# Kernel tuning notes

Measured on AMD Instinct MI355X. Metric: run time of the kernel, lower is better.

Reference implementation:

```python
import jax, jax.numpy as jnp
import numpy as np

EPS = 1e-5
GROUPS = 16


def _deform_conv_gn(input, offset, mask, weight, bias, gamma, beta):
    # Modulated deformable conv v2 (k=3, stride=1, pad=1) + GroupNorm(16).
    B, C, H, W = input.shape
    Co = weight.shape[0]
    K = 9
    # kernel taps relative to center (pad=1 cancels the -1 origin shift)
    ky = jnp.repeat(jnp.arange(3) - 1, 3).astype(input.dtype)   # [9]
    kx = jnp.tile(jnp.arange(3) - 1, 3).astype(input.dtype)     # [9]
    off = offset.reshape(B, K, 2, H, W)                          # (dy, dx) per tap
    dy, dx = off[:, :, 0], off[:, :, 1]                          # [B,9,H,W]
    y = jnp.arange(H, dtype=input.dtype)[None, None, :, None] + ky[None, :, None, None] + dy
    x = jnp.arange(W, dtype=input.dtype)[None, None, None, :] + kx[None, :, None, None] + dx
    y0 = jnp.floor(y)
    x0 = jnp.floor(x)
    flat = input.reshape(B, C, H * W)

    def corner(yc, xc):
        # zero-padded bilinear corner gather -> [B,C,9,H,W]
        valid = ((yc >= 0) & (yc < H) & (xc >= 0) & (xc < W)).astype(input.dtype)
        yi = jnp.clip(yc, 0, H - 1).astype(jnp.int32)
        xi = jnp.clip(xc, 0, W - 1).astype(jnp.int32)
        idx = (yi * W + xi).reshape(B, -1)
        g = jax.vmap(lambda im, ix: jnp.take(im, ix, axis=1))(flat, idx)
        return g.reshape(B, C, K, H, W) * valid[:, None]

    wy1 = y - y0
    wx1 = x - x0
    wy0 = 1.0 - wy1
    wx0 = 1.0 - wx1
    val = (corner(y0, x0) * (wy0 * wx0)[:, None]
           + corner(y0, x0 + 1.0) * (wy0 * wx1)[:, None]
           + corner(y0 + 1.0, x0) * (wy1 * wx0)[:, None]
           + corner(y0 + 1.0, x0 + 1.0) * (wy1 * wx1)[:, None])
    cols = val * mask[:, None]                                   # modulation [B,C,9,H,W]
    out = jnp.einsum('bckhw,ock->bohw', cols, weight.reshape(Co, C, K))
    out = out + bias[None, :, None, None]
    # GroupNorm(16)
    g = out.reshape(B, GROUPS, Co // GROUPS, H, W)
    mu = g.mean(axis=(2, 3, 4), keepdims=True)
    var = g.var(axis=(2, 3, 4), keepdims=True)
    g = (g - mu) * jax.lax.rsqrt(var + EPS)
    return g.reshape(B, Co, H, W) * gamma[None, :, None, None] + beta[None, :, None, None]


def setup_inputs() -> dict:
    key = jax.random.key(0)
    k1, k2, k3, k4 = jax.random.split(key, 4)
    B, C, Co, H, W = 4, 256, 256, 64, 64
    return {
        'input': jax.random.normal(k1, (B, C, H, W), dtype=jnp.float32),
        'offset': jax.random.normal(k2, (B, 18, H, W), dtype=jnp.float32),
        'mask': jax.random.uniform(k3, (B, 9, H, W), dtype=jnp.float32),
        'weight': jax.random.normal(k4, (Co, C, 3, 3), dtype=jnp.float32) * 0.02,
        'bias': jnp.zeros((Co,), dtype=jnp.float32),
        'gamma': jnp.ones((Co,), dtype=jnp.float32),
        'beta': jnp.zeros((Co,), dtype=jnp.float32),
    }


def reference(input, offset, mask, weight, bias, gamma, beta):
    return _deform_conv_gn(input, offset, mask, weight, bias, gamma, beta)
```

## Files before the change

### kernel.cpp

```cpp
#include <hip/hip_runtime.h>

typedef __attribute__((ext_vector_type(8))) short short8;
typedef __attribute__((ext_vector_type(4))) float f32x4;

#define Bsz 4
#define Cin 256
#define Cout 256
#define Hh 64
#define Ww 64
#define HW 4096
#define NG 16
#define EPSV 1e-5f

#define CSTR 40

static __device__ __forceinline__ unsigned f2bf(float f) {
    unsigned u = __float_as_uint(f);
    return (u + 0x7fffu + ((u >> 16) & 1u)) >> 16;
}

static __device__ __forceinline__ float2 ld8(const float* p) {
    float2 v;
    __builtin_memcpy(&v, p, 8);
    return v;
}

__global__ void wt_kernel(const float* __restrict__ w, ushort* __restrict__ wtb,
                          float* __restrict__ stats) {
    const int i = blockIdx.x * 256 + threadIdx.x;
    if (blockIdx.x == 0 && threadIdx.x < 128) stats[threadIdx.x] = 0.f;
    if (i >= Cout * Cin * 9) return;
    const int o = i / (Cin * 9);
    const int rem = i % (Cin * 9);
    const int c = rem / 9, kk = rem % 9;
    const int ks = kk * 8 + (c >> 5);
    wtb[(ks * 256 + o) * 32 + (c & 31)] = (ushort)f2bf(w[i]);
}

__launch_bounds__(512, 2)
__global__ void dcn_kernel(const float* __restrict__ in,
                           const float* __restrict__ offs,
                           const float* __restrict__ mask,
                           const ushort* __restrict__ wtb,
                           const float* __restrict__ bias,
                           float* __restrict__ out,
                           float* __restrict__ stats) {
    __shared__ int2   s_ta[9 * 64];
    __shared__ float4 s_tw[9 * 64];
    __shared__ ushort s_col[2][64 * CSTR];

    const int t  = threadIdx.x;
    const int bx = blockIdx.x;
    const int q  = bx & 7, r = bx >> 3;
    const int b  = q >> 1;
    const int h  = ((q & 1) << 5) | r;
    const int lane = t & 63;
    const int wv   = t >> 6;
    const int n    = lane;
    const int quad = lane >> 4;
    const int l15  = lane & 15;

    for (int j = t; j < 576; j += 512) {
        const int k = j >> 6, p = j & 63;
        const float* ob = offs + (size_t)b * 18 * HW + h * Ww + p;
        const float dy = ob[(2 * k) * HW];
        const float dx = ob[(2 * k + 1) * HW];
        const float m  = mask[((size_t)b * 9 + k) * HW + h * Ww + p];
        const float y = (float)h + (float)(k / 3 - 1) + dy;
        const float x = (float)p + (float)(k % 3 - 1) + dx;
        const float y0f = floorf(y), x0f = floorf(x);
        const float ly = y - y0f, lx = x - x0f;
        const float hy = 1.f - ly, hx = 1.f - lx;
        const int y0 = (int)y0f, x0 = (int)x0f;
        const int yc0 = min(max(y0, 0), 63);
        const int yc1 = min(max(y0 + 1, 0), 63);
        const int xb  = min(max(x0, 0), 62);
        float ax = 0.f, ay = 0.f;
        if (x0 == xb) {
            ax = hx;
            ay = lx;
        } else if (x0 < xb) {
            ax = (x0 + 1 == 0) ? lx : 0.f;
        } else {
            ay = (x0 == 63) ? hx : 0.f;
        }
        const float w0 = (y0 >= 0 && y0 < 64) ? m * hy : 0.f;
        const float w1 = (y0 + 1 >= 0 && y0 + 1 < 64) ? m * ly : 0.f;
        s_ta[j] = make_int2(yc0 * 64 + xb, yc1 * 64 + xb);
        s_tw[j] = make_float4(w0 * ax, w0 * ay, w1 * ax, w1 * ay);
    }
    __syncthreads();

    f32x4 acc[2][4];
#pragma unroll
    for (int i = 0; i < 2; i++)
#pragma unroll
        for (int nt = 0; nt < 4; nt++) acc[i][nt] = (f32x4){0.f, 0.f, 0.f, 0.f};

    const float* inb = in + (size_t)b * Cin * HW;

#define GATHER(cc, kk, pk0, pk1)                                           \
    {                                                                      \
        const int2  ad = s_ta[(kk) * 64 + n];                              \
        const float4 tw = s_tw[(kk) * 64 + n];                             \
        const float* cb = inb + (size_t)((cc) * 32 + wv * 4) * HW;         \
        float vv[4];                                                       \
        _Pragma("unroll")                                                  \
        for (int j = 0; j < 4; j++) {                                      \
            const float* pl = cb + j * HW;                                 \
            const float2 g0 = ld8(pl + ad.x);                              \
            const float2 g1 = ld8(pl + ad.y);                              \
            vv[j] = tw.x * g0.x + tw.y * g0.y + tw.z * g1.x + tw.w * g1.y; \
        }                                                                  \
        pk0 = f2bf(vv[0]) | (f2bf(vv[1]) << 16);                           \
        pk1 = f2bf(vv[2]) | (f2bf(vv[3]) << 16);                           \
    }

    unsigned pk0, pk1;
    GATHER(0, 0, pk0, pk1);

    int p = 0;
#pragma unroll 1
    for (int s = 0; s < 72; s++) {
        const int cc = s / 9;
        const int kk = s - cc * 9;
        const int ks = kk * 8 + cc;
        *(unsigned long long*)&s_col[p][n * CSTR + wv * 4] =
            (unsigned long long)pk0 | ((unsigned long long)pk1 << 32);
        __syncthreads();
        if (s < 71) {
            const int s1 = s + 1;
            const int cc1 = s1 / 9;
            GATHER(cc1, s1 - cc1 * 9, pk0, pk1);
        }
        const ushort* wp = wtb + ((size_t)(ks * 256 + wv * 32 + l15)) * 32 + quad * 8;
        const short8 a0 = *(const short8*)wp;
        const short8 a1 = *(const short8*)(wp + 16 * 32);
        short8 bfr[4];
#pragma unroll
        for (int nt = 0; nt < 4; nt++)
            bfr[nt] = *(const short8*)&s_col[p][(nt * 16 + l15) * CSTR + quad * 8];
#pragma unroll
        for (int nt = 0; nt < 4; nt++) {
            acc[0][nt] = __builtin_amdgcn_mfma_f32_16x16x32_bf16(a0, bfr[nt], acc[0][nt], 0, 0, 0);
            acc[1][nt] = __builtin_amdgcn_mfma_f32_16x16x32_bf16(a1, bfr[nt], acc[1][nt], 0, 0, 0);
        }
        p ^= 1;
    }
#undef GATHER

    float gs[2], gq[2];
#pragma unroll
    for (int i = 0; i < 2; i++) {
        float s = 0.f, qq = 0.f;
        const int ob = wv * 32 + i * 16 + quad * 4;
#pragma unroll
        for (int reg = 0; reg < 4; reg++) {
            const int o = ob + reg;
            const float bv = bias[o];
            float* op = out + ((size_t)(b * 256 + o)) * HW + h * Ww + l15;
#pragma unroll
            for (int nt = 0; nt < 4; nt++) {
                const float v = acc[i][nt][reg] + bv;
                op[nt * 16] = v;
                s += v;
                qq += v * v;
            }
        }
        gs[i] = s; gq[i] = qq;
    }
#pragma unroll
    for (int off = 32; off; off >>= 1) {
        gs[0] += __shfl_xor(gs[0], off);
        gq[0] += __shfl_xor(gq[0], off);
        gs[1] += __shfl_xor(gs[1], off);
        gq[1] += __shfl_xor(gq[1], off);
    }
    if (lane == 0) {
#pragma unroll
        for (int i = 0; i < 2; i++) {
            const int g = wv * 2 + i;
            atomicAdd(&stats[((size_t)b * NG + g) * 2],     gs[i]);
            atomicAdd(&stats[((size_t)b * NG + g) * 2 + 1], gq[i]);
        }
    }
}

__global__ void gn_apply_kernel(float* __restrict__ x, const float* __restrict__ stats,
                                const float* __restrict__ gamma,
                                const float* __restrict__ beta) {
    const int i = blockIdx.x * 256 + threadIdx.x;
    const int plane = i >> 10;
    const int o = plane & 255;
    const int bg = plane >> 4;
    const float s = stats[bg * 2], q = stats[bg * 2 + 1];
    const float inv_n = 1.f / 65536.f;
    const float mu = s * inv_n;
    const float var = q * inv_n - mu * mu;
    const float rs = rsqrtf(var + EPSV);
    const float ga = gamma[o] * rs;
    const float be = beta[o] - mu * ga;
    float4 v = ((float4*)x)[i];
    v.x = v.x * ga + be;
    v.y = v.y * ga + be;
    v.z = v.z * ga + be;
    v.w = v.w * ga + be;
    ((float4*)x)[i] = v;
}

extern "C" void kernel_launch(void* const* d_in, const int* in_sizes, int n_in,
                              void* d_out, int out_size, void* d_ws, size_t ws_size,
                              hipStream_t stream) {
    const float* input  = (const float*)d_in[0];
    const float* offset = (const float*)d_in[1];
    const float* maskp  = (const float*)d_in[2];
    const float* weight = (const float*)d_in[3];
    const float* bias   = (const float*)d_in[4];
    const float* gamma  = (const float*)d_in[5];
    const float* beta   = (const float*)d_in[6];
    float* out = (float*)d_out;

    ushort* wtb  = (ushort*)d_ws;
    float* stats = (float*)((char*)d_ws + (size_t)Cout * Cin * 9 * sizeof(ushort));

    hipLaunchKernelGGL(wt_kernel, dim3((Cout * Cin * 9 + 255) / 256), dim3(256), 0,
                       stream, weight, wtb, stats);
    hipLaunchKernelGGL(dcn_kernel, dim3(Bsz * Hh), dim3(512), 0, stream,
                       input, offset, maskp, wtb, bias, out, stats);
    hipLaunchKernelGGL(gn_apply_kernel, dim3((Bsz * Cout * HW / 4) / 256), dim3(256), 0,
                       stream, out, stats, gamma, beta);
}
```

Before: 217.3 us.

## Split each row into half-width tiles, doubling blocks; write weights coalesced

The main kernel now gives each block a 32-pixel half row instead of a full 64-pixel row, so twice as many blocks launch (512 rather than 256). Launch bounds are raised to 4 blocks per SM so more of them can be resident. The aim is to fill the GPU's compute units better and hide gather latency. The cost is that every weight tile now gets reloaded for half the pixels, which doubles weight traffic per output. The weight-transpose kernel is also rewritten to index by output position, so its writes are coalesced.

Result: slower. 233.2 us (+7.3%).

```diff
diff --git a/kernel.cpp b/kernel.cpp
--- a/kernel.cpp
+++ b/kernel.cpp
@@ -29,15 +29,16 @@
                           float* __restrict__ stats) {
     const int i = blockIdx.x * 256 + threadIdx.x;
     if (blockIdx.x == 0 && threadIdx.x < 128) stats[threadIdx.x] = 0.f;
-    if (i >= Cout * Cin * 9) return;
-    const int o = i / (Cin * 9);
-    const int rem = i % (Cin * 9);
-    const int c = rem / 9, kk = rem % 9;
-    const int ks = kk * 8 + (c >> 5);
-    wtb[(ks * 256 + o) * 32 + (c & 31)] = (ushort)f2bf(w[i]);
-}
-
-__launch_bounds__(512, 2)
+    if (i >= 72 * 256 * 32) return;
+    const int cl = i & 31;
+    const int o  = (i >> 5) & 255;
+    const int ks = i >> 13;
+    const int c  = ((ks & 7) << 5) | cl;
+    const int kk = ks >> 3;
+    wtb[i] = (ushort)f2bf(w[((size_t)o * Cin + c) * 9 + kk]);
+}
+
+__launch_bounds__(512, 4)
 __global__ void dcn_kernel(const float* __restrict__ in,
                            const float* __restrict__ offs,
                            const float* __restrict__ mask,
@@ -45,29 +46,31 @@
                            const float* __restrict__ bias,
                            float* __restrict__ out,
                            float* __restrict__ stats) {
-    __shared__ int2   s_ta[9 * 64];
-    __shared__ float4 s_tw[9 * 64];
-    __shared__ ushort s_col[2][64 * CSTR];
+    __shared__ int2   s_ta[9 * 32];
+    __shared__ float4 s_tw[9 * 32];
+    __shared__ ushort s_col[2][32 * CSTR];
 
     const int t  = threadIdx.x;
     const int bx = blockIdx.x;
     const int q  = bx & 7, r = bx >> 3;
     const int b  = q >> 1;
-    const int h  = ((q & 1) << 5) | r;
+    const int h  = ((q & 1) << 5) | (r >> 1);
+    const int wb = (r & 1) << 5;
     const int lane = t & 63;
     const int wv   = t >> 6;
-    const int n    = lane;
+    const int px   = lane & 31;
+    const int hi   = lane >> 5;
     const int quad = lane >> 4;
     const int l15  = lane & 15;
 
-    for (int j = t; j < 576; j += 512) {
-        const int k = j >> 6, p = j & 63;
-        const float* ob = offs + (size_t)b * 18 * HW + h * Ww + p;
+    for (int j = t; j < 288; j += 512) {
+        const int k = j >> 5, p = j & 31;
+        const float* ob = offs + (size_t)b * 18 * HW + h * Ww + wb + p;
         const float dy = ob[(2 * k) * HW];
         const float dx = ob[(2 * k + 1) * HW];
-        const float m  = mask[((size_t)b * 9 + k) * HW + h * Ww + p];
+        const float m  = mask[((size_t)b * 9 + k) * HW + h * Ww + wb + p];
         const float y = (float)h + (float)(k / 3 - 1) + dy;
-        const float x = (float)p + (float)(k % 3 - 1) + dx;
+        const float x = (float)(wb + p) + (float)(k % 3 - 1) + dx;
         const float y0f = floorf(y), x0f = floorf(x);
         const float ly = y - y0f, lx = x - x0f;
         const float hy = 1.f - ly, hx = 1.f - lx;
@@ -91,33 +94,32 @@
     }
     __syncthreads();
 
-    f32x4 acc[2][4];
+    f32x4 acc[2][2];
 #pragma unroll
     for (int i = 0; i < 2; i++)
 #pragma unroll
-        for (int nt = 0; nt < 4; nt++) acc[i][nt] = (f32x4){0.f, 0.f, 0.f, 0.f};
+        for (int nt = 0; nt < 2; nt++) acc[i][nt] = (f32x4){0.f, 0.f, 0.f, 0.f};
 
     const float* inb = in + (size_t)b * Cin * HW;
 
-#define GATHER(cc, kk, pk0, pk1)                                           \
+#define GATHER(cc, kk, pk)                                                 \
     {                                                                      \
-        const int2  ad = s_ta[(kk) * 64 + n];                              \
-        const float4 tw = s_tw[(kk) * 64 + n];                             \
-        const float* cb = inb + (size_t)((cc) * 32 + wv * 4) * HW;         \
-        float vv[4];                                                       \
+        const int2  ad = s_ta[(kk) * 32 + px];                             \
+        const float4 tw = s_tw[(kk) * 32 + px];                            \
+        const float* cb = inb + (size_t)((cc) * 32 + wv * 4 + hi * 2) * HW;\
+        float vv[2];                                                       \
         _Pragma("unroll")                                                  \
-        for (int j = 0; j < 4; j++) {                                      \
+        for (int j = 0; j < 2; j++) {                                      \
             const float* pl = cb + j * HW;                                 \
             const float2 g0 = ld8(pl + ad.x);                              \
             const float2 g1 = ld8(pl + ad.y);                              \
             vv[j] = tw.x * g0.x + tw.y * g0.y + tw.z * g1.x + tw.w * g1.y; \
         }                                                                  \
-        pk0 = f2bf(vv[0]) | (f2bf(vv[1]) << 16);                           \
-        pk1 = f2bf(vv[2]) | (f2bf(vv[3]) << 16);                           \
-    }
-
-    unsigned pk0, pk1;
-    GATHER(0, 0, pk0, pk1);
+        pk = f2bf(vv[0]) | (f2bf(vv[1]) << 16);                           \
+    }
+
+    unsigned pk;
+    GATHER(0, 0, pk);
 
     int p = 0;
 #pragma unroll 1
@@ -125,23 +127,22 @@
         const int cc = s / 9;
         const int kk = s - cc * 9;
         const int ks = kk * 8 + cc;
-        *(unsigned long long*)&s_col[p][n * CSTR + wv * 4] =
-            (unsigned long long)pk0 | ((unsigned long long)pk1 << 32);
+        *(unsigned*)&s_col[p][px * CSTR + wv * 4 + hi * 2] = pk;
         __syncthreads();
         if (s < 71) {
             const int s1 = s + 1;
             const int cc1 = s1 / 9;
-            GATHER(cc1, s1 - cc1 * 9, pk0, pk1);
+            GATHER(cc1, s1 - cc1 * 9, pk);
         }
         const ushort* wp = wtb + ((size_t)(ks * 256 + wv * 32 + l15)) * 32 + quad * 8;
         const short8 a0 = *(const short8*)wp;
         const short8 a1 = *(const short8*)(wp + 16 * 32);
-        short8 bfr[4];
-#pragma unroll
-        for (int nt = 0; nt < 4; nt++)
+        short8 bfr[2];
+#pragma unroll
+        for (int nt = 0; nt < 2; nt++)
             bfr[nt] = *(const short8*)&s_col[p][(nt * 16 + l15) * CSTR + quad * 8];
 #pragma unroll
-        for (int nt = 0; nt < 4; nt++) {
+        for (int nt = 0; nt < 2; nt++) {
             acc[0][nt] = __builtin_amdgcn_mfma_f32_16x16x32_bf16(a0, bfr[nt], acc[0][nt], 0, 0, 0);
             acc[1][nt] = __builtin_amdgcn_mfma_f32_16x16x32_bf16(a1, bfr[nt], acc[1][nt], 0, 0, 0);
         }
@@ -158,9 +159,9 @@
         for (int reg = 0; reg < 4; reg++) {
             const int o = ob + reg;
             const float bv = bias[o];
-            float* op = out + ((size_t)(b * 256 + o)) * HW + h * Ww + l15;
-#pragma unroll
-            for (int nt = 0; nt < 4; nt++) {
+            float* op = out + ((size_t)(b * 256 + o)) * HW + h * Ww + wb + l15;
+#pragma unroll
+            for (int nt = 0; nt < 2; nt++) {
                 const float v = acc[i][nt][reg] + bv;
                 op[nt * 16] = v;
                 s += v;
@@ -225,7 +226,7 @@
 
     hipLaunchKernelGGL(wt_kernel, dim3((Cout * Cin * 9 + 255) / 256), dim3(256), 0,
                        stream, weight, wtb, stats);
-    hipLaunchKernelGGL(dcn_kernel, dim3(Bsz * Hh), dim3(512), 0, stream,
+    hipLaunchKernelGGL(dcn_kernel, dim3(Bsz * Hh * 2), dim3(512), 0, stream,
                        input, offset, maskp, wtb, bias, out, stats);
     hipLaunchKernelGGL(gn_apply_kernel, dim3((Bsz * Cout * HW / 4) / 256), dim3(256), 0,
                        stream, out, stats, gamma, beta);
```

## Stage input row band in LDS for deformable gathers, coalesce weight repack

Applied to the files above, without the earlier changes.

Each block computes the min and max source row touched by its bilinear samples. When that range fits in 16 rows, it copies the 32-channel slab of those rows into LDS with global_load_lds at each channel-chunk boundary, and the bilinear gathers then read from LDS instead of scattered global memory. A fallback keeps the old global-gather path for wide offset ranges. The weight-repack kernel is also rewritten so its bf16 writes are contiguous. The cost is roughly 150KB of dynamic LDS, which limits the kernel to one block per CU, plus an extra barrier and a non-overlapped staging step at every chunk boundary.

Result: faster. 190.8 us (-12.2%).

```diff
diff --git a/kernel.cpp b/kernel.cpp
--- a/kernel.cpp
+++ b/kernel.cpp
@@ -13,6 +13,19 @@
 #define EPSV 1e-5f
 
 #define CSTR 40
+#define SPAN 16
+#define PLF (SPAN*64)
+
+#define OFF_IN   0
+#define SZ_IN    (32 * PLF * 4)
+#define OFF_COL  (OFF_IN + SZ_IN)
+#define SZ_COL   (2 * 64 * CSTR * 2)
+#define OFF_TA   (OFF_COL + SZ_COL)
+#define SZ_TA    (576 * 8)
+#define OFF_TW   (OFF_TA + SZ_TA)
+#define SZ_TW    (576 * 16)
+#define OFF_CTL  (OFF_TW + SZ_TW)
+#define SMEM_BYTES (OFF_CTL + 16)
 
 static __device__ __forceinline__ unsigned f2bf(float f) {
     unsigned u = __float_as_uint(f);
@@ -29,15 +42,16 @@
                           float* __restrict__ stats) {
     const int i = blockIdx.x * 256 + threadIdx.x;
     if (blockIdx.x == 0 && threadIdx.x < 128) stats[threadIdx.x] = 0.f;
-    if (i >= Cout * Cin * 9) return;
-    const int o = i / (Cin * 9);
-    const int rem = i % (Cin * 9);
-    const int c = rem / 9, kk = rem % 9;
-    const int ks = kk * 8 + (c >> 5);
-    wtb[(ks * 256 + o) * 32 + (c & 31)] = (ushort)f2bf(w[i]);
-}
-
-__launch_bounds__(512, 2)
+    if (i >= 72 * 256 * 32) return;
+    const int cl = i & 31;
+    const int o  = (i >> 5) & 255;
+    const int ks = i >> 13;
+    const int c  = ((ks & 7) << 5) | cl;
+    const int kk = ks >> 3;
+    wtb[i] = (ushort)f2bf(w[((size_t)o * Cin + c) * 9 + kk]);
+}
+
+__launch_bounds__(512, 1)
 __global__ void dcn_kernel(const float* __restrict__ in,
                            const float* __restrict__ offs,
                            const float* __restrict__ mask,
@@ -45,9 +59,12 @@
                            const float* __restrict__ bias,
                            float* __restrict__ out,
                            float* __restrict__ stats) {
-    __shared__ int2   s_ta[9 * 64];
-    __shared__ float4 s_tw[9 * 64];
-    __shared__ ushort s_col[2][64 * CSTR];
+    extern __shared__ char smem[];
+    float*  s_in = (float*)(smem + OFF_IN);
+    ushort* col  = (ushort*)(smem + OFF_COL);
+    int2*   s_ta = (int2*)(smem + OFF_TA);
+    float4* s_tw = (float4*)(smem + OFF_TW);
+    int*    s_ctl = (int*)(smem + OFF_CTL);
 
     const int t  = threadIdx.x;
     const int bx = blockIdx.x;
@@ -60,14 +77,18 @@
     const int quad = lane >> 4;
     const int l15  = lane & 15;
 
+    if (t < 2) s_ctl[t] = (t == 0) ? 64 : -1;
+    __syncthreads();
+
+    int my_min = 64, my_max = -1;
     for (int j = t; j < 576; j += 512) {
-        const int k = j >> 6, p = j & 63;
-        const float* ob = offs + (size_t)b * 18 * HW + h * Ww + p;
+        const int k = j >> 6, pp = j & 63;
+        const float* ob = offs + (size_t)b * 18 * HW + h * Ww + pp;
         const float dy = ob[(2 * k) * HW];
         const float dx = ob[(2 * k + 1) * HW];
-        const float m  = mask[((size_t)b * 9 + k) * HW + h * Ww + p];
+        const float m  = mask[((size_t)b * 9 + k) * HW + h * Ww + pp];
         const float y = (float)h + (float)(k / 3 - 1) + dy;
-        const float x = (float)p + (float)(k % 3 - 1) + dx;
+        const float x = (float)pp + (float)(k % 3 - 1) + dx;
         const float y0f = floorf(y), x0f = floorf(x);
         const float ly = y - y0f, lx = x - x0f;
         const float hy = 1.f - ly, hx = 1.f - lx;
@@ -88,9 +109,24 @@
         const float w1 = (y0 + 1 >= 0 && y0 + 1 < 64) ? m * ly : 0.f;
         s_ta[j] = make_int2(yc0 * 64 + xb, yc1 * 64 + xb);
         s_tw[j] = make_float4(w0 * ax, w0 * ay, w1 * ax, w1 * ay);
+        my_min = min(my_min, yc0);
+        my_max = max(my_max, yc1);
+    }
+#pragma unroll
+    for (int off = 32; off; off >>= 1) {
+        my_min = min(my_min, __shfl_xor(my_min, off));
+        my_max = max(my_max, __shfl_xor(my_max, off));
+    }
+    if (lane == 0) {
+        atomicMin(&s_ctl[0], my_min);
+        atomicMax(&s_ctl[1], my_max);
     }
     __syncthreads();
 
+    const int ymin = s_ctl[0];
+    const bool use_lds = (s_ctl[1] - ymin + 1) <= SPAN;
+    const int ymin64 = ymin << 6;
+
     f32x4 acc[2][4];
 #pragma unroll
     for (int i = 0; i < 2; i++)
@@ -99,7 +135,43 @@
 
     const float* inb = in + (size_t)b * Cin * HW;
 
-#define GATHER(cc, kk, pk0, pk1)                                           \
+#define STAGE(cc)                                                              \
+    {                                                                          \
+        const float* cbs = inb + (size_t)((cc) * 32) * HW;                     \
+        _Pragma("unroll")                                                      \
+        for (int i = 0; i < 16; i++) {                                         \
+            const int g = (wv << 4) | i;                                       \
+            const int plane = g >> 2;                                          \
+            const int row = min(ymin + ((g & 3) << 2) + (lane >> 4), 63);      \
+            const float* src = cbs + (size_t)plane * HW + row * 64 +           \
+                               ((lane & 15) << 2);                             \
+            __builtin_amdgcn_global_load_lds(                                  \
+                (const __attribute__((address_space(1))) void*)src,            \
+                (__attribute__((address_space(3))) void*)(smem + OFF_IN +      \
+                                                          g * 1024),          \
+                16, 0, 0);                                                     \
+        }                                                                      \
+    }
+
+#define GATHER_L(kk, pk0, pk1)                                             \
+    {                                                                      \
+        const int2  ad = s_ta[(kk) * 64 + n];                              \
+        const float4 tw = s_tw[(kk) * 64 + n];                             \
+        const int r0 = ad.x - ymin64, r1 = ad.y - ymin64;                  \
+        const float* cb = s_in + (wv << 2) * PLF;                          \
+        float vv[4];                                                       \
+        _Pragma("unroll")                                                  \
+        for (int j = 0; j < 4; j++) {                                      \
+            const float* pl = cb + j * PLF;                                \
+            const float2 g0 = ld8(pl + r0);                                \
+            const float2 g1 = ld8(pl + r1);                                \
+            vv[j] = tw.x * g0.x + tw.y * g0.y + tw.z * g1.x + tw.w * g1.y; \
+        }                                                                  \
+        pk0 = f2bf(vv[0]) | (f2bf(vv[1]) << 16);                           \
+        pk1 = f2bf(vv[2]) | (f2bf(vv[3]) << 16);                           \
+    }
+
+#define GATHER_G(cc, kk, pk0, pk1)                                         \
     {                                                                      \
         const int2  ad = s_ta[(kk) * 64 + n];                              \
         const float4 tw = s_tw[(kk) * 64 + n];                             \
@@ -116,38 +188,77 @@
         pk1 = f2bf(vv[2]) | (f2bf(vv[3]) << 16);                           \
     }
 
+#define FRAGS_MFMA(ks, p)                                                      \
+    {                                                                          \
+        const ushort* wp =                                                     \
+            wtb + ((size_t)((ks) * 256 + wv * 32 + l15)) * 32 + quad * 8;      \
+        const short8 a0 = *(const short8*)wp;                                  \
+        const short8 a1 = *(const short8*)(wp + 16 * 32);                      \
+        short8 bfr[4];                                                         \
+        _Pragma("unroll")                                                      \
+        for (int nt = 0; nt < 4; nt++)                                         \
+            bfr[nt] = *(const short8*)&col[(p) * (64 * CSTR) +                 \
+                                           (nt * 16 + l15) * CSTR + quad * 8]; \
+        _Pragma("unroll")                                                      \
+        for (int nt = 0; nt < 4; nt++) {                                       \
+            acc[0][nt] = __builtin_amdgcn_mfma_f32_16x16x32_bf16(              \
+                a0, bfr[nt], acc[0][nt], 0, 0, 0);                             \
+            acc[1][nt] = __builtin_amdgcn_mfma_f32_16x16x32_bf16(              \
+                a1, bfr[nt], acc[1][nt], 0, 0, 0);                             \
+        }                                                                      \
+    }
+
     unsigned pk0, pk1;
-    GATHER(0, 0, pk0, pk1);
-
     int p = 0;
+
+    if (use_lds) {
+        STAGE(0);
+        __syncthreads();
+        GATHER_L(0, pk0, pk1);
 #pragma unroll 1
-    for (int s = 0; s < 72; s++) {
-        const int cc = s / 9;
-        const int kk = s - cc * 9;
-        const int ks = kk * 8 + cc;
-        *(unsigned long long*)&s_col[p][n * CSTR + wv * 4] =
-            (unsigned long long)pk0 | ((unsigned long long)pk1 << 32);
-        __syncthreads();
-        if (s < 71) {
-            const int s1 = s + 1;
-            const int cc1 = s1 / 9;
-            GATHER(cc1, s1 - cc1 * 9, pk0, pk1);
-        }
-        const ushort* wp = wtb + ((size_t)(ks * 256 + wv * 32 + l15)) * 32 + quad * 8;
-        const short8 a0 = *(const short8*)wp;
-        const short8 a1 = *(const short8*)(wp + 16 * 32);
-        short8 bfr[4];
-#pragma unroll
-        for (int nt = 0; nt < 4; nt++)
-            bfr[nt] = *(const short8*)&s_col[p][(nt * 16 + l15) * CSTR + quad * 8];
-#pragma unroll
-        for (int nt = 0; nt < 4; nt++) {
-            acc[0][nt] = __builtin_amdgcn_mfma_f32_16x16x32_bf16(a0, bfr[nt], acc[0][nt], 0, 0, 0);
-            acc[1][nt] = __builtin_amdgcn_mfma_f32_16x16x32_bf16(a1, bfr[nt], acc[1][nt], 0, 0, 0);
-        }
-        p ^= 1;
-    }
-#undef GATHER
+        for (int s = 0; s < 72; s++) {
+            const int cc = s / 9;
+            const int kk = s - cc * 9;
+            const int ks = kk * 8 + cc;
+            *(unsigned long long*)&col[p * (64 * CSTR) + n * CSTR + (wv << 2)] =
+                (unsigned long long)pk0 | ((unsigned long long)pk1 << 32);
+            __syncthreads();
+            const bool bound = (kk == 8) && (s != 71);
+            if (bound) {
+                STAGE(cc + 1);
+            } else if (s != 71) {
+                GATHER_L(kk + 1, pk0, pk1);
+            }
+            FRAGS_MFMA(ks, p);
+            if (bound) {
+                __syncthreads();
+                GATHER_L(0, pk0, pk1);
+            }
+            p ^= 1;
+        }
+    } else {
+        GATHER_G(0, 0, pk0, pk1);
+#pragma unroll 1
+        for (int s = 0; s < 72; s++) {
+            const int cc = s / 9;
+            const int kk = s - cc * 9;
+            const int ks = kk * 8 + cc;
+            *(unsigned long long*)&col[p * (64 * CSTR) + n * CSTR + (wv << 2)] =
+                (unsigned long long)pk0 | ((unsigned long long)pk1 << 32);
+            __syncthreads();
+            if (s < 71) {
+                const int s1 = s + 1;
+                const int cc1 = s1 / 9;
+                GATHER_G(cc1, s1 - cc1 * 9, pk0, pk1);
+            }
+            FRAGS_MFMA(ks, p);
+            p ^= 1;
+        }
+    }
+#undef STAGE
+#undef GATHER_L
+#undef GATHER_G
+#undef FRAGS_MFMA
 
     float gs[2], gq[2];
 #pragma unroll
@@ -223,9 +334,16 @@
     ushort* wtb  = (ushort*)d_ws;
     float* stats = (float*)((char*)d_ws + (size_t)Cout * Cin * 9 * sizeof(ushort));
 
+    static int attr_done = 0;
+    if (!attr_done) {
+        hipFuncSetAttribute((const void*)dcn_kernel,
+                            hipFuncAttributeMaxDynamicSharedMemorySize, SMEM_BYTES);
+        attr_done = 1;
+    }
+
     hipLaunchKernelGGL(wt_kernel, dim3((Cout * Cin * 9 + 255) / 256), dim3(256), 0,
                        stream, weight, wtb, stats);
-    hipLaunchKernelGGL(dcn_kernel, dim3(Bsz * Hh), dim3(512), 0, stream,
+    hipLaunchKernelGGL(dcn_kernel, dim3(Bsz * Hh), dim3(512), SMEM_BYTES, stream,
                        input, offset, maskp, wtb, bias, out, stats);
     hipLaunchKernelGGL(gn_apply_kernel, dim3((Bsz * Cout * HW / 4) / 256), dim3(256), 0,
                        stream, out, stats, gamma, beta);
```
